# Optimization experiments

Measured on AMD Instinct MI355X. Metric: run time of the kernel, lower is better.

The kernel has to match this reference:

```python
import jax, jax.numpy as jnp
import numpy as np

COST_CLASS = 2.0
COST_MASK = 5.0
COST_DICE = 5.0
NUM_POINTS = 12544


def _point_sample(masks, coords):
    """Bilinear sample masks [N,H,W] at coords [P,2] in [0,1] (x,y order),
    matching F.grid_sample(align_corners=False, padding_mode='zeros')."""
    H, W = masks.shape[-2], masks.shape[-1]
    x = coords[:, 0] * W - 0.5  # [P]
    y = coords[:, 1] * H - 0.5
    x0 = jnp.floor(x)
    y0 = jnp.floor(y)
    wx = (x - x0).astype(masks.dtype)
    wy = (y - y0).astype(masks.dtype)
    x0i = x0.astype(jnp.int32)
    y0i = y0.astype(jnp.int32)

    def gather(xi, yi):
        valid = ((xi >= 0) & (xi < W) & (yi >= 0) & (yi < H)).astype(masks.dtype)
        xc = jnp.clip(xi, 0, W - 1)
        yc = jnp.clip(yi, 0, H - 1)
        return masks[:, yc, xc] * valid[None, :]  # [N,P]

    v00 = gather(x0i, y0i)
    v01 = gather(x0i + 1, y0i)
    v10 = gather(x0i, y0i + 1)
    v11 = gather(x0i + 1, y0i + 1)
    return (v00 * (1 - wx) * (1 - wy) + v01 * wx * (1 - wy)
            + v10 * (1 - wx) * wy + v11 * wx * wy)  # [N,P]


def setup_inputs() -> dict:
    key = jax.random.key(0)
    ks = jax.random.split(key, 6)
    B, Q, C, T, H, W = 8, 100, 41, 50, 256, 256
    return {
        "pred_logits": jax.random.normal(ks[0], (B, Q, C), jnp.float32),
        "pred_object_logits": jax.random.normal(ks[1], (B, Q, 2), jnp.float32),
        "pred_masks": jax.random.normal(ks[2], (B, Q, H, W), jnp.float32),
        "tgt_masks": jax.random.uniform(ks[3], (B, T, H, W), jnp.float32),
        "tgt_labels": jax.random.randint(ks[4], (B, T), 0, C),
        "point_coords": jax.random.uniform(ks[5], (B, NUM_POINTS, 2), jnp.float32),
    }


def reference(pred_logits, pred_object_logits, pred_masks, tgt_masks, tgt_labels, point_coords):
    B, Q, C = pred_logits.shape
    T = tgt_labels.shape[1]
    P = point_coords.shape[1]

    # --- class cost ---
    out_class_prob = jax.nn.sigmoid(pred_logits[..., :-1])          # [B,Q,C-1]
    out_object_prob = jax.nn.softmax(pred_object_logits, axis=-1)   # [B,Q,2]
    out_prob = jnp.concatenate(
        [jnp.sqrt(out_class_prob * out_object_prob[..., 0:1]),
         out_object_prob[..., 1:2]], axis=-1)                       # [B,Q,C]
    idx = jnp.broadcast_to(tgt_labels[:, None, :], (B, Q, T))
    cost_class = -jnp.take_along_axis(out_prob, idx, axis=2)        # [B,Q,T]

    # --- point-sample masks at shared random points ---
    om = jax.vmap(_point_sample)(pred_masks, point_coords)          # [B,Q,P]
    tm = jax.vmap(_point_sample)(tgt_masks, point_coords)           # [B,T,P]

    # --- batched sigmoid CE cost ---
    pos = jax.nn.softplus(-om)  # BCE vs target=1
    neg = jax.nn.softplus(om)   # BCE vs target=0
    cost_mask = (jnp.einsum('bqp,btp->bqt', pos, tm)
                 + jnp.einsum('bqp,btp->bqt', neg, 1.0 - tm)) / P

    # --- batched dice cost ---
    s = jax.nn.sigmoid(om)
    numerator = 2.0 * jnp.einsum('bqp,btp->bqt', s, tm)
    denominator = s.sum(-1)[:, :, None] + tm.sum(-1)[:, None, :]
    cost_dice = 1.0 - (numerator + 1.0) / (denominator + 1.0)

    Cmat = COST_MASK * cost_mask + COST_CLASS * cost_class + COST_DICE * cost_dice
    return Cmat  # [B,Q,T] batched assignment cost matrices
```

## Files before the change

### kernel.cpp

```cpp
#include <hip/hip_runtime.h>
#include <math.h>

#define BB 8
#define QQ 100
#define CC 41
#define TT 50
#define PP 12544
#define QP 112
#define TP 64
#define KS 8
#define KCH (PP / KS)
#define NT (BB * TT)
#define NMASK (NT + BB * QQ)
#define MPB 5
#define SGRID (NMASK / MPB)

typedef _Float16 f16x8 __attribute__((ext_vector_type(8)));
typedef float f32x4 __attribute__((ext_vector_type(4)));

#if defined(__has_builtin)
#if __has_builtin(__builtin_amdgcn_cvt_pk_fp8_f32) && __has_builtin(__builtin_amdgcn_cvt_f32_fp8)
#define HAVE_FP8CVT 1
#endif
#endif

__device__ __forceinline__ unsigned int cvt1_e4m3_sw(float x) {
    unsigned int u = __float_as_uint(x);
    unsigned int s = (u >> 24) & 0x80u;
    float ax = fminf(fabsf(x), 448.f);
    if (ax < 0.015625f) {
        unsigned int m = (unsigned int)rintf(ax * 512.f);
        return s | m;
    }
    unsigned int v = __float_as_uint(ax);
    v += 0x7FFFFu + ((v >> 20) & 1u);
    int e = (int)(v >> 23) - 127;
    unsigned int m = (v >> 20) & 7u;
    if (e < -6) { m = (unsigned int)rintf(ax * 512.f); return s | m; }
    unsigned int ee = (unsigned int)(e + 7);
    if (ee >= 16u) { ee = 15u; m = 6u; }
    return s | (ee << 3) | m;
}

template <bool HI>
__device__ __forceinline__ unsigned int pack2_e4m3(float a, float b, unsigned int old) {
#ifdef HAVE_FP8CVT
    return (unsigned int)__builtin_amdgcn_cvt_pk_fp8_f32(a, b, (int)old, HI);
#else
    unsigned int p = (cvt1_e4m3_sw(a) | (cvt1_e4m3_sw(b) << 8)) << (HI ? 16 : 0);
    unsigned int mask = HI ? 0x0000FFFFu : 0xFFFF0000u;
    return (old & mask) | p;
#endif
}

__device__ __forceinline__ float e4m3_to_f32(unsigned int byte) {
#ifdef HAVE_FP8CVT
    return __builtin_amdgcn_cvt_f32_fp8((int)byte, 0);
#else
    unsigned int s = byte >> 7, e = (byte >> 3) & 15u, m = byte & 7u;
    float v = e ? __uint_as_float(((e + 120u) << 23) | (m << 20))
                : (float)m * 0.001953125f;
    return s ? -v : v;
#endif
}

__device__ __forceinline__ void addr_w(float2 c, int& a00, int& a01, int& a10, int& a11,
                                       float& xa, float& xb, float& ya, float& yb) {
    float x = fmaf(c.x, 256.f, -0.5f);
    float y = fmaf(c.y, 256.f, -0.5f);
    float x0f = floorf(x), y0f = floorf(y);
    float wx = x - x0f, wy = y - y0f;
    int x0 = (int)x0f, y0 = (int)y0f;
    float fx0 = (x0 >= 0) ? 1.f : 0.f, fx1 = (x0 < 255) ? 1.f : 0.f;
    float fy0 = (y0 >= 0) ? 1.f : 0.f, fy1 = (y0 < 255) ? 1.f : 0.f;
    int x0c = max(x0, 0), x1c = min(x0 + 1, 255);
    int r0 = max(y0, 0) << 8, r1 = min(y0 + 1, 255) << 8;
    a00 = r0 + x0c; a01 = r0 + x1c; a10 = r1 + x0c; a11 = r1 + x1c;
    xa = (1.f - wx) * fx0; xb = wx * fx1;
    ya = (1.f - wy) * fy0; yb = wy * fy1;
}

__global__ __launch_bounds__(1024, 4) void sample_kernel(
    const float* __restrict__ tgt_masks, const float* __restrict__ pred_masks,
    const float* __restrict__ coords,
    _Float16* __restrict__ tm, _Float16* __restrict__ om, _Float16* __restrict__ sg,
    float* __restrict__ tmsum, float* __restrict__ nsum, float* __restrict__ ssum)
{
    __shared__ unsigned int buf[2][16384];
    __shared__ float red[16], red2[16];
    int tid = threadIdx.x;
    int base = blockIdx.x * MPB;

    {
        const float* m0 = (base < NT) ? tgt_masks + (size_t)base * 65536
                                      : pred_masks + (size_t)(base - NT) * 65536;
        const float4* s4 = (const float4*)m0;
        for (int half = 0; half < 2; ++half) {
            float4 r[8];
            #pragma unroll
            for (int k = 0; k < 8; ++k) r[k] = s4[half * 8192 + k * 1024 + tid];
            #pragma unroll
            for (int k = 0; k < 8; ++k) {
                unsigned int pk = pack2_e4m3<false>(r[k].x, r[k].y, 0u);
                buf[0][half * 8192 + k * 1024 + tid] = pack2_e4m3<true>(r[k].z, r[k].w, pk);
            }
        }
    }
    __syncthreads();

    for (int j = 0; j < MPB; ++j) {
        int id = base + j;
        bool is_t = id < NT;
        int b;
        _Float16* dst;
        _Float16* dsg = nullptr;
        if (is_t) {
            b = id / TT;
            dst = tm + ((size_t)b * TP + (id % TT)) * PP;
        } else {
            int bq = id - NT;
            b = bq / QQ;
            dst = om + ((size_t)b * QP + (bq % QQ)) * PP;
            dsg = sg + ((size_t)b * QP + (bq % QQ)) * PP;
        }
        const float2* cd = (const float2*)coords + (size_t)b * PP;
        const unsigned char* curb = (const unsigned char*)buf[j & 1];
        unsigned int* nxt = buf[(j + 1) & 1];
        bool has_next = (j + 1 < MPB);
        const float4* ns4 = nullptr;
        if (has_next) {
            int nid = id + 1;
            ns4 = (const float4*)((nid < NT) ? tgt_masks + (size_t)nid * 65536
                                             : pred_masks + (size_t)(nid - NT) * 65536);
        }

        float l1 = 0.f, l2 = 0.f;
        for (int half = 0; half < 2; ++half) {
            float4 r[8];
            if (has_next) {
                #pragma unroll
                for (int k = 0; k < 8; ++k) r[k] = ns4[half * 8192 + k * 1024 + tid];
            }
            #pragma unroll
            for (int pr = 0; pr < 3; ++pr) {
                int p1 = (half * 6 + pr * 2) * 1024 + tid;
                int p2 = p1 + 1024;
                float2 c1 = cd[p1], c2 = cd[p2];
                int a00, a01, a10, a11, e00, e01, e10, e11;
                float xa1, xb1, ya1, yb1, xa2, xb2, ya2, yb2;
                addr_w(c1, a00, a01, a10, a11, xa1, xb1, ya1, yb1);
                addr_w(c2, e00, e01, e10, e11, xa2, xb2, ya2, yb2);
                unsigned int u00 = curb[a00], u01 = curb[a01];
                unsigned int u10 = curb[a10], u11 = curb[a11];
                unsigned int w00 = curb[e00], w01 = curb[e01];
                unsigned int w10 = curb[e10], w11 = curb[e11];
                float v1 = ya1 * fmaf(xa1, e4m3_to_f32(u00), xb1 * e4m3_to_f32(u01))
                         + yb1 * fmaf(xa1, e4m3_to_f32(u10), xb1 * e4m3_to_f32(u11));
                float v2 = ya2 * fmaf(xa2, e4m3_to_f32(w00), xb2 * e4m3_to_f32(w01))
                         + yb2 * fmaf(xa2, e4m3_to_f32(w10), xb2 * e4m3_to_f32(w11));
                dst[p1] = (_Float16)v1;
                dst[p2] = (_Float16)v2;
                if (is_t) {
                    l1 += v1 + v2;
                } else {
                    float e1 = __expf(-fabsf(v1)), e2 = __expf(-fabsf(v2));
                    float q1 = 1.f / (1.f + e1), q2 = 1.f / (1.f + e2);
                    float g1 = (v1 >= 0.f) ? q1 : e1 * q1;
                    float g2 = (v2 >= 0.f) ? q2 : e2 * q2;
                    dsg[p1] = (_Float16)g1;
                    dsg[p2] = (_Float16)g2;
                    l1 += fmaxf(v1, 0.f) + __logf(1.f + e1)
                        + fmaxf(v2, 0.f) + __logf(1.f + e2);
                    l2 += g1 + g2;
                }
            }
            if (half == 1 && tid < 256) {
                int p = 12288 + tid;
                float2 c = cd[p];
                int a00, a01, a10, a11;
                float xa, xb, ya, yb;
                addr_w(c, a00, a01, a10, a11, xa, xb, ya, yb);
                float v = ya * fmaf(xa, e4m3_to_f32((unsigned int)curb[a00]),
                                    xb * e4m3_to_f32((unsigned int)curb[a01]))
                        + yb * fmaf(xa, e4m3_to_f32((unsigned int)curb[a10]),
                                    xb * e4m3_to_f32((unsigned int)curb[a11]));
                dst[p] = (_Float16)v;
                if (is_t) {
                    l1 += v;
                } else {
                    float e = __expf(-fabsf(v));
                    float q = 1.f / (1.f + e);
                    float g = (v >= 0.f) ? q : e * q;
                    dsg[p] = (_Float16)g;
                    l1 += fmaxf(v, 0.f) + __logf(1.f + e);
                    l2 += g;
                }
            }
            if (has_next) {
                #pragma unroll
                for (int k = 0; k < 8; ++k) {
                    unsigned int pk = pack2_e4m3<false>(r[k].x, r[k].y, 0u);
                    nxt[half * 8192 + k * 1024 + tid] = pack2_e4m3<true>(r[k].z, r[k].w, pk);
                }
            }
        }

        #pragma unroll
        for (int off = 32; off; off >>= 1) {
            l1 += __shfl_down(l1, off, 64);
            l2 += __shfl_down(l2, off, 64);
        }
        if ((tid & 63) == 0) { red[tid >> 6] = l1; red2[tid >> 6] = l2; }
        __syncthreads();
        if (tid == 0) {
            float t1 = 0.f, t2 = 0.f;
            #pragma unroll
            for (int w = 0; w < 16; ++w) { t1 += red[w]; t2 += red2[w]; }
            if (is_t) tmsum[id] = t1;
            else { nsum[id - NT] = t1; ssum[id - NT] = t2; }
        }
        __syncthreads();
    }
}

__global__ __launch_bounds__(256) void dot_mfma_kernel(
    const _Float16* __restrict__ om, const _Float16* __restrict__ sg,
    const _Float16* __restrict__ tm,
    float* __restrict__ part_om, float* __restrict__ part_s)
{
    int qt = blockIdx.x, b = blockIdx.y, ks = blockIdx.z;
    int tid = threadIdx.x, lane = tid & 63, w = tid >> 6;
    int ra = lane & 15;
    int ko = (lane >> 4) * 8;
    const _Float16* pa = om + ((size_t)(b * QP + qt * 16 + ra)) * PP + ks * KCH + ko;
    const _Float16* ps = sg + ((size_t)(b * QP + qt * 16 + ra)) * PP + ks * KCH + ko;
    const _Float16* pb = tm + ((size_t)(b * TP + w * 16 + ra)) * PP + ks * KCH + ko;
    f32x4 accO = {0.f, 0.f, 0.f, 0.f};
    f32x4 accS = {0.f, 0.f, 0.f, 0.f};
    #pragma unroll 7
    for (int k = 0; k < KCH / 32; ++k) {
        f16x8 a = *(const f16x8*)(pa + (size_t)k * 32);
        f16x8 s = *(const f16x8*)(ps + (size_t)k * 32);
        f16x8 bb = *(const f16x8*)(pb + (size_t)k * 32);
        accO = __builtin_amdgcn_mfma_f32_16x16x32_f16(a, bb, accO, 0, 0, 0);
        accS = __builtin_amdgcn_mfma_f32_16x16x32_f16(s, bb, accS, 0, 0, 0);
    }
    int t = w * 16 + ra;
    int q = qt * 16 + (lane >> 4) * 4;
    size_t bse = (((size_t)ks * BB + b) * QP + q) * TP + t;
    #pragma unroll
    for (int r = 0; r < 4; ++r) {
        part_om[bse + (size_t)r * TP] = accO[r];
        part_s[bse + (size_t)r * TP] = accS[r];
    }
}

__global__ __launch_bounds__(256) void epilogue_kernel(
    const float* __restrict__ part_om, const float* __restrict__ part_s,
    const float* __restrict__ tmsum, const float* __restrict__ nsum,
    const float* __restrict__ ssum, const float* __restrict__ pred_logits,
    const float* __restrict__ pred_obj, const int* __restrict__ labels,
    float* __restrict__ out)
{
    int i = blockIdx.x * 256 + threadIdx.x;
    if (i >= BB * QQ * TT) return;
    int t = i % TT;
    int bq = i / TT;
    int b = bq / QQ, q = bq % QQ;
    float dO = 0.f, dS = 0.f;
    #pragma unroll
    for (int ks = 0; ks < KS; ++ks) {
        size_t o = (((size_t)ks * BB + b) * QP + q) * TP + t;
        dO += part_om[o];
        dS += part_s[o];
    }
    float ns = nsum[bq], ss = ssum[bq];
    float ts = tmsum[b * TT + t];
    float cmask = (ns - dO) * (1.f / PP);
    float cdice = 1.f - (2.f * dS + 1.f) / (ss + ts + 1.f);
    int label = labels[b * TT + t];
    float a0 = pred_obj[bq * 2], a1 = pred_obj[bq * 2 + 1];
    float prob;
    if (label == CC - 1) {
        prob = 1.f / (1.f + __expf(a0 - a1));
    } else {
        float pc = 1.f / (1.f + __expf(-pred_logits[(size_t)bq * CC + label]));
        float po = 1.f / (1.f + __expf(a1 - a0));
        prob = sqrtf(pc * po);
    }
    out[i] = 5.f * cmask - 2.f * prob + 5.f * cdice;
}

extern "C" void kernel_launch(void* const* d_in, const int* in_sizes, int n_in,
                              void* d_out, int out_size, void* d_ws, size_t ws_size,
                              hipStream_t stream) {
    const float* pred_logits = (const float*)d_in[0];
    const float* pred_obj    = (const float*)d_in[1];
    const float* pred_masks  = (const float*)d_in[2];
    const float* tgt_masks   = (const float*)d_in[3];
    const int*   tgt_labels  = (const int*)d_in[4];
    const float* coords      = (const float*)d_in[5];
    float* out = (float*)d_out;

    char* ws = (char*)d_ws;
    const size_t SZ_OM = (size_t)BB * QP * PP * 2;
    const size_t SZ_TM = (size_t)BB * TP * PP * 2;
    const size_t SZ_PT = (size_t)KS * BB * QP * TP * 4;
    _Float16* om  = (_Float16*)ws;
    _Float16* sg  = (_Float16*)(ws + SZ_OM);
    _Float16* tmm = (_Float16*)(ws + 2 * SZ_OM);
    float* part_om = (float*)(ws + 2 * SZ_OM + SZ_TM);
    float* part_s  = (float*)(ws + 2 * SZ_OM + SZ_TM + SZ_PT);
    float* tmsum   = (float*)(ws + 2 * SZ_OM + SZ_TM + 2 * SZ_PT);
    float* nsum    = tmsum + BB * TT;
    float* ssum    = nsum + BB * QQ;

    hipLaunchKernelGGL(sample_kernel, dim3(SGRID), dim3(1024), 0, stream,
                       tgt_masks, pred_masks, coords, tmm, om, sg, tmsum, nsum, ssum);
    hipLaunchKernelGGL(dot_mfma_kernel, dim3(QP / 16, BB, KS), dim3(256), 0, stream,
                       om, sg, tmm, part_om, part_s);
    hipLaunchKernelGGL(epilogue_kernel, dim3((BB * QQ * TT + 255) / 256), dim3(256),
                       0, stream,
                       part_om, part_s, tmsum, nsum, ssum,
                       pred_logits, pred_obj, tgt_labels, out);
}
```

Measured before the change: 124.4 us.

## Precompute bilinear address/weight table and sample one mask per block

Adds a kernel that precomputes, per batch and point, the four packed 16-bit LDS addresses and fp16 bilinear corner weights. The sampling kernel reads this table instead of recomputing floor and clamp math for every mask. It also drops the 5-masks-per-block double-buffered pipeline in favour of one mask per block with a single 64KB LDS buffer and higher occupancy, and packs f16 output stores in pairs. The cost is an extra launch plus 16B of table traffic per point per mask, fp16 weight rounding, and no intra-block overlap of mask loading with sampling.

```diff
diff --git a/kernel.cpp b/kernel.cpp
--- a/kernel.cpp
+++ b/kernel.cpp
@@ -12,8 +12,6 @@
 #define KCH (PP / KS)
 #define NT (BB * TT)
 #define NMASK (NT + BB * QQ)
-#define MPB 5
-#define SGRID (NMASK / MPB)
 
 typedef _Float16 f16x8 __attribute__((ext_vector_type(8)));
 typedef float f32x4 __attribute__((ext_vector_type(4)));
@@ -64,8 +62,12 @@
 #endif
 }
 
-__device__ __forceinline__ void addr_w(float2 c, int& a00, int& a01, int& a10, int& a11,
-                                       float& xa, float& xb, float& ya, float& yb) {
+__global__ __launch_bounds__(256) void table_kernel(
+    const float* __restrict__ coords, uint4* __restrict__ table)
+{
+    int i = blockIdx.x * 256 + threadIdx.x;
+    if (i >= BB * PP) return;
+    float2 c = ((const float2*)coords)[i];
     float x = fmaf(c.x, 256.f, -0.5f);
     float y = fmaf(c.y, 256.f, -0.5f);
     float x0f = floorf(x), y0f = floorf(y);
@@ -73,153 +75,163 @@
     int x0 = (int)x0f, y0 = (int)y0f;
     float fx0 = (x0 >= 0) ? 1.f : 0.f, fx1 = (x0 < 255) ? 1.f : 0.f;
     float fy0 = (y0 >= 0) ? 1.f : 0.f, fy1 = (y0 < 255) ? 1.f : 0.f;
-    int x0c = max(x0, 0), x1c = min(x0 + 1, 255);
-    int r0 = max(y0, 0) << 8, r1 = min(y0 + 1, 255) << 8;
-    a00 = r0 + x0c; a01 = r0 + x1c; a10 = r1 + x0c; a11 = r1 + x1c;
-    xa = (1.f - wx) * fx0; xb = wx * fx1;
-    ya = (1.f - wy) * fy0; yb = wy * fy1;
-}
-
-__global__ __launch_bounds__(1024, 4) void sample_kernel(
+    unsigned int x0c = (unsigned int)max(x0, 0), x1c = (unsigned int)min(x0 + 1, 255);
+    unsigned int r0 = ((unsigned int)max(y0, 0)) << 8;
+    unsigned int r1 = ((unsigned int)min(y0 + 1, 255)) << 8;
+    float xa = (1.f - wx) * fx0, xb = wx * fx1;
+    float ya = (1.f - wy) * fy0, yb = wy * fy1;
+    union { unsigned int u; _Float16 h[2]; } w1, w2;
+    w1.h[0] = (_Float16)(xa * ya); w1.h[1] = (_Float16)(xb * ya);
+    w2.h[0] = (_Float16)(xa * yb); w2.h[1] = (_Float16)(xb * yb);
+    uint4 t;
+    t.x = (r0 + x0c) | ((r0 + x1c) << 16);
+    t.y = (r1 + x0c) | ((r1 + x1c) << 16);
+    t.z = w1.u; t.w = w2.u;
+    table[i] = t;
+}
+
+__device__ __forceinline__ float tbl_interp(const unsigned char* __restrict__ mlds, uint4 t) {
+    float v00 = e4m3_to_f32(mlds[t.x & 0xffffu]);
+    float v01 = e4m3_to_f32(mlds[t.x >> 16]);
+    float v10 = e4m3_to_f32(mlds[t.y & 0xffffu]);
+    float v11 = e4m3_to_f32(mlds[t.y >> 16]);
+    union { unsigned int u; _Float16 h[2]; } w1, w2;
+    w1.u = t.z; w2.u = t.w;
+    float acc = (float)w1.h[0] * v00;
+    acc = fmaf((float)w1.h[1], v01, acc);
+    acc = fmaf((float)w2.h[0], v10, acc);
+    return fmaf((float)w2.h[1], v11, acc);
+}
+
+__global__ __launch_bounds__(1024, 8) void sample_kernel(
     const float* __restrict__ tgt_masks, const float* __restrict__ pred_masks,
-    const float* __restrict__ coords,
+    const uint4* __restrict__ table,
     _Float16* __restrict__ tm, _Float16* __restrict__ om, _Float16* __restrict__ sg,
     float* __restrict__ tmsum, float* __restrict__ nsum, float* __restrict__ ssum)
 {
-    __shared__ unsigned int buf[2][16384];
+    __shared__ unsigned char mlds[65536];
     __shared__ float red[16], red2[16];
+    int id = blockIdx.x;
     int tid = threadIdx.x;
-    int base = blockIdx.x * MPB;
+    bool is_t = id < NT;
+    int b;
+    _Float16* dst;
+    _Float16* dsg = nullptr;
+    const float* m;
+    if (is_t) {
+        b = id / TT;
+        m = tgt_masks + (size_t)id * 65536;
+        dst = tm + ((size_t)b * TP + (id % TT)) * PP;
+    } else {
+        int bq = id - NT;
+        b = bq / QQ;
+        m = pred_masks + (size_t)bq * 65536;
+        dst = om + ((size_t)b * QP + (bq % QQ)) * PP;
+        dsg = sg + ((size_t)b * QP + (bq % QQ)) * PP;
+    }
+    const uint4* tb = table + (size_t)b * PP;
 
     {
-        const float* m0 = (base < NT) ? tgt_masks + (size_t)base * 65536
-                                      : pred_masks + (size_t)(base - NT) * 65536;
-        const float4* s4 = (const float4*)m0;
-        for (int half = 0; half < 2; ++half) {
-            float4 r[8];
-            #pragma unroll
-            for (int k = 0; k < 8; ++k) r[k] = s4[half * 8192 + k * 1024 + tid];
-            #pragma unroll
-            for (int k = 0; k < 8; ++k) {
-                unsigned int pk = pack2_e4m3<false>(r[k].x, r[k].y, 0u);
-                buf[0][half * 8192 + k * 1024 + tid] = pack2_e4m3<true>(r[k].z, r[k].w, pk);
-            }
+        const float4* s4 = (const float4*)m;
+        unsigned int* dl = (unsigned int*)mlds;
+        #pragma unroll
+        for (int bt = 0; bt < 4; ++bt) {
+            float4 r0 = s4[bt * 4096 + tid];
+            float4 r1 = s4[bt * 4096 + 1024 + tid];
+            float4 r2 = s4[bt * 4096 + 2048 + tid];
+            float4 r3 = s4[bt * 4096 + 3072 + tid];
+            unsigned int pk;
+            pk = pack2_e4m3<false>(r0.x, r0.y, 0u);
+            dl[bt * 4096 + tid] = pack2_e4m3<true>(r0.z, r0.w, pk);
+            pk = pack2_e4m3<false>(r1.x, r1.y, 0u);
+            dl[bt * 4096 + 1024 + tid] = pack2_e4m3<true>(r1.z, r1.w, pk);
+            pk = pack2_e4m3<false>(r2.x, r2.y, 0u);
+            dl[bt * 4096 + 2048 + tid] = pack2_e4m3<true>(r2.z, r2.w, pk);
+            pk = pack2_e4m3<false>(r3.x, r3.y, 0u);
+            dl[bt * 4096 + 3072 + tid] = pack2_e4m3<true>(r3.z, r3.w, pk);
         }
     }
     __syncthreads();
 
-    for (int j = 0; j < MPB; ++j) {
-        int id = base + j;
-        bool is_t = id < NT;
-        int b;
-        _Float16* dst;
-        _Float16* dsg = nullptr;
-        if (is_t) {
-            b = id / TT;
-            dst = tm + ((size_t)b * TP + (id % TT)) * PP;
-        } else {
-            int bq = id - NT;
-            b = bq / QQ;
-            dst = om + ((size_t)b * QP + (bq % QQ)) * PP;
-            dsg = sg + ((size_t)b * QP + (bq % QQ)) * PP;
-        }
-        const float2* cd = (const float2*)coords + (size_t)b * PP;
-        const unsigned char* curb = (const unsigned char*)buf[j & 1];
-        unsigned int* nxt = buf[(j + 1) & 1];
-        bool has_next = (j + 1 < MPB);
-        const float4* ns4 = nullptr;
-        if (has_next) {
-            int nid = id + 1;
-            ns4 = (const float4*)((nid < NT) ? tgt_masks + (size_t)nid * 65536
-                                             : pred_masks + (size_t)(nid - NT) * 65536);
-        }
-
-        float l1 = 0.f, l2 = 0.f;
-        for (int half = 0; half < 2; ++half) {
-            float4 r[8];
-            if (has_next) {
-                #pragma unroll
-                for (int k = 0; k < 8; ++k) r[k] = ns4[half * 8192 + k * 1024 + tid];
-            }
-            #pragma unroll
-            for (int pr = 0; pr < 3; ++pr) {
-                int p1 = (half * 6 + pr * 2) * 1024 + tid;
-                int p2 = p1 + 1024;
-                float2 c1 = cd[p1], c2 = cd[p2];
-                int a00, a01, a10, a11, e00, e01, e10, e11;
-                float xa1, xb1, ya1, yb1, xa2, xb2, ya2, yb2;
-                addr_w(c1, a00, a01, a10, a11, xa1, xb1, ya1, yb1);
-                addr_w(c2, e00, e01, e10, e11, xa2, xb2, ya2, yb2);
-                unsigned int u00 = curb[a00], u01 = curb[a01];
-                unsigned int u10 = curb[a10], u11 = curb[a11];
-                unsigned int w00 = curb[e00], w01 = curb[e01];
-                unsigned int w10 = curb[e10], w11 = curb[e11];
-                float v1 = ya1 * fmaf(xa1, e4m3_to_f32(u00), xb1 * e4m3_to_f32(u01))
-                         + yb1 * fmaf(xa1, e4m3_to_f32(u10), xb1 * e4m3_to_f32(u11));
-                float v2 = ya2 * fmaf(xa2, e4m3_to_f32(w00), xb2 * e4m3_to_f32(w01))
-                         + yb2 * fmaf(xa2, e4m3_to_f32(w10), xb2 * e4m3_to_f32(w11));
-                dst[p1] = (_Float16)v1;
-                dst[p2] = (_Float16)v2;
-                if (is_t) {
-                    l1 += v1 + v2;
-                } else {
-                    float e1 = __expf(-fabsf(v1)), e2 = __expf(-fabsf(v2));
-                    float q1 = 1.f / (1.f + e1), q2 = 1.f / (1.f + e2);
-                    float g1 = (v1 >= 0.f) ? q1 : e1 * q1;
-                    float g2 = (v2 >= 0.f) ? q2 : e2 * q2;
-                    dsg[p1] = (_Float16)g1;
-                    dsg[p2] = (_Float16)g2;
-                    l1 += fmaxf(v1, 0.f) + __logf(1.f + e1)
-                        + fmaxf(v2, 0.f) + __logf(1.f + e2);
-                    l2 += g1 + g2;
-                }
-            }
-            if (half == 1 && tid < 256) {
-                int p = 12288 + tid;
-                float2 c = cd[p];
-                int a00, a01, a10, a11;
-                float xa, xb, ya, yb;
-                addr_w(c, a00, a01, a10, a11, xa, xb, ya, yb);
-                float v = ya * fmaf(xa, e4m3_to_f32((unsigned int)curb[a00]),
-                                    xb * e4m3_to_f32((unsigned int)curb[a01]))
-                        + yb * fmaf(xa, e4m3_to_f32((unsigned int)curb[a10]),
-                                    xb * e4m3_to_f32((unsigned int)curb[a11]));
-                dst[p] = (_Float16)v;
-                if (is_t) {
-                    l1 += v;
-                } else {
-                    float e = __expf(-fabsf(v));
-                    float q = 1.f / (1.f + e);
-                    float g = (v >= 0.f) ? q : e * q;
-                    dsg[p] = (_Float16)g;
-                    l1 += fmaxf(v, 0.f) + __logf(1.f + e);
-                    l2 += g;
-                }
-            }
-            if (has_next) {
-                #pragma unroll
-                for (int k = 0; k < 8; ++k) {
-                    unsigned int pk = pack2_e4m3<false>(r[k].x, r[k].y, 0u);
-                    nxt[half * 8192 + k * 1024 + tid] = pack2_e4m3<true>(r[k].z, r[k].w, pk);
-                }
-            }
-        }
-
+    float l1 = 0.f, l2 = 0.f;
+
+    if (is_t) {
         #pragma unroll
-        for (int off = 32; off; off >>= 1) {
-            l1 += __shfl_down(l1, off, 64);
-            l2 += __shfl_down(l2, off, 64);
-        }
-        if ((tid & 63) == 0) { red[tid >> 6] = l1; red2[tid >> 6] = l2; }
-        __syncthreads();
-        if (tid == 0) {
-            float t1 = 0.f, t2 = 0.f;
-            #pragma unroll
-            for (int w = 0; w < 16; ++w) { t1 += red[w]; t2 += red2[w]; }
-            if (is_t) tmsum[id] = t1;
-            else { nsum[id - NT] = t1; ssum[id - NT] = t2; }
-        }
-        __syncthreads();
+        for (int g = 0; g < 6; ++g) {
+            int p = g * 2048 + 2 * tid;
+            uint4 t0 = tb[p], t1 = tb[p + 1];
+            float v1 = tbl_interp(mlds, t0);
+            float v2 = tbl_interp(mlds, t1);
+            union { unsigned int u; _Float16 h[2]; } o;
+            o.h[0] = (_Float16)v1; o.h[1] = (_Float16)v2;
+            *(unsigned int*)&dst[p] = o.u;
+            l1 += v1 + v2;
+        }
+        if (tid < 128) {
+            int p = 12288 + 2 * tid;
+            uint4 t0 = tb[p], t1 = tb[p + 1];
+            float v1 = tbl_interp(mlds, t0);
+            float v2 = tbl_interp(mlds, t1);
+            union { unsigned int u; _Float16 h[2]; } o;
+            o.h[0] = (_Float16)v1; o.h[1] = (_Float16)v2;
+            *(unsigned int*)&dst[p] = o.u;
+            l1 += v1 + v2;
+        }
+    } else {
+        #pragma unroll
+        for (int g = 0; g < 6; ++g) {
+            int p = g * 2048 + 2 * tid;
+            uint4 t0 = tb[p], t1 = tb[p + 1];
+            float v1 = tbl_interp(mlds, t0);
+            float v2 = tbl_interp(mlds, t1);
+            union { unsigned int u; _Float16 h[2]; } o;
+            o.h[0] = (_Float16)v1; o.h[1] = (_Float16)v2;
+            *(unsigned int*)&dst[p] = o.u;
+            float e1 = __expf(-fabsf(v1)), e2 = __expf(-fabsf(v2));
+            float q1 = 1.f / (1.f + e1), q2 = 1.f / (1.f + e2);
+            float g1 = (v1 >= 0.f) ? q1 : e1 * q1;
+            float g2 = (v2 >= 0.f) ? q2 : e2 * q2;
+            union { unsigned int u; _Float16 h[2]; } os;
+            os.h[0] = (_Float16)g1; os.h[1] = (_Float16)g2;
+            *(unsigned int*)&dsg[p] = os.u;
+            l1 += fmaxf(v1, 0.f) + __logf(1.f + e1)
+                + fmaxf(v2, 0.f) + __logf(1.f + e2);
+            l2 += g1 + g2;
+        }
+        if (tid < 128) {
+            int p = 12288 + 2 * tid;
+            uint4 t0 = tb[p], t1 = tb[p + 1];
+            float v1 = tbl_interp(mlds, t0);
+            float v2 = tbl_interp(mlds, t1);
+            union { unsigned int u; _Float16 h[2]; } o;
+            o.h[0] = (_Float16)v1; o.h[1] = (_Float16)v2;
+            *(unsigned int*)&dst[p] = o.u;
+            float e1 = __expf(-fabsf(v1)), e2 = __expf(-fabsf(v2));
+            float q1 = 1.f / (1.f + e1), q2 = 1.f / (1.f + e2);
+            float g1 = (v1 >= 0.f) ? q1 : e1 * q1;
+            float g2 = (v2 >= 0.f) ? q2 : e2 * q2;
+            union { unsigned int u; _Float16 h[2]; } os;
+            os.h[0] = (_Float16)g1; os.h[1] = (_Float16)g2;
+            *(unsigned int*)&dsg[p] = os.u;
+            l1 += fmaxf(v1, 0.f) + __logf(1.f + e1)
+                + fmaxf(v2, 0.f) + __logf(1.f + e2);
+            l2 += g1 + g2;
+        }
+    }
+
+    #pragma unroll
+    for (int off = 32; off; off >>= 1) {
+        l1 += __shfl_down(l1, off, 64);
+        l2 += __shfl_down(l2, off, 64);
+    }
+    if ((tid & 63) == 0) { red[tid >> 6] = l1; red2[tid >> 6] = l2; }
+    __syncthreads();
+    if (tid == 0) {
+        float t1 = 0.f, t2 = 0.f;
+        #pragma unroll
+        for (int w = 0; w < 16; ++w) { t1 += red[w]; t2 += red2[w]; }
+        if (is_t) tmsum[id] = t1;
+        else { nsum[id - NT] = t1; ssum[id - NT] = t2; }
     }
 }
 
@@ -303,20 +315,24 @@
     float* out = (float*)d_out;
 
     char* ws = (char*)d_ws;
+    const size_t SZ_TB = (size_t)BB * PP * 16;
     const size_t SZ_OM = (size_t)BB * QP * PP * 2;
     const size_t SZ_TM = (size_t)BB * TP * PP * 2;
     const size_t SZ_PT = (size_t)KS * BB * QP * TP * 4;
-    _Float16* om  = (_Float16*)ws;
-    _Float16* sg  = (_Float16*)(ws + SZ_OM);
-    _Float16* tmm = (_Float16*)(ws + 2 * SZ_OM);
-    float* part_om = (float*)(ws + 2 * SZ_OM + SZ_TM);
-    float* part_s  = (float*)(ws + 2 * SZ_OM + SZ_TM + SZ_PT);
-    float* tmsum   = (float*)(ws + 2 * SZ_OM + SZ_TM + 2 * SZ_PT);
+    uint4* table  = (uint4*)ws;
+    _Float16* om  = (_Float16*)(ws + SZ_TB);
+    _Float16* sg  = (_Float16*)(ws + SZ_TB + SZ_OM);
+    _Float16* tmm = (_Float16*)(ws + SZ_TB + 2 * SZ_OM);
+    float* part_om = (float*)(ws + SZ_TB + 2 * SZ_OM + SZ_TM);
+    float* part_s  = (float*)(ws + SZ_TB + 2 * SZ_OM + SZ_TM + SZ_PT);
+    float* tmsum   = (float*)(ws + SZ_TB + 2 * SZ_OM + SZ_TM + 2 * SZ_PT);
     float* nsum    = tmsum + BB * TT;
     float* ssum    = nsum + BB * QQ;
 
-    hipLaunchKernelGGL(sample_kernel, dim3(SGRID), dim3(1024), 0, stream,
-                       tgt_masks, pred_masks, coords, tmm, om, sg, tmsum, nsum, ssum);
+    hipLaunchKernelGGL(table_kernel, dim3((BB * PP + 255) / 256), dim3(256), 0, stream,
+                       coords, table);
+    hipLaunchKernelGGL(sample_kernel, dim3(NMASK), dim3(1024), 0, stream,
+                       tgt_masks, pred_masks, table, tmm, om, sg, tmsum, nsum, ssum);
     hipLaunchKernelGGL(dot_mfma_kernel, dim3(QP / 16, BB, KS), dim3(256), 0, stream,
                        om, sg, tmm, part_om, part_s);
     hipLaunchKernelGGL(epilogue_kernel, dim3((BB * QQ * TT + 255) / 256), dim3(256),
```

New measurement: 124.4 us. About the same (-0.0%).

## Precompute row-binned bilinear sample table and gather masks directly from global memory

Applied to the files above, without the earlier changes.

A new sort_kernel bins each batch's sample points by source row band and writes a compact table with clamped addresses and fp16 bilinear weights. The sample kernel then runs one block per mask and gathers four fp32 texels per point straight from global memory, instead of staging the whole mask into LDS as fp8. This removes the fp8 packing, the double-buffered LDS staging and the per-point address math, and also raises sampling precision. Row binning is meant to improve cache locality of the gathers. The cost is an extra kernel launch and a serialized ballot-compaction loop. Point order is permuted, which the downstream permutation-invariant reductions tolerate.

```diff
diff --git a/kernel.cpp b/kernel.cpp
--- a/kernel.cpp
+++ b/kernel.cpp
@@ -12,214 +12,142 @@
 #define KCH (PP / KS)
 #define NT (BB * TT)
 #define NMASK (NT + BB * QQ)
-#define MPB 5
-#define SGRID (NMASK / MPB)
 
 typedef _Float16 f16x8 __attribute__((ext_vector_type(8)));
 typedef float f32x4 __attribute__((ext_vector_type(4)));
 
-#if defined(__has_builtin)
-#if __has_builtin(__builtin_amdgcn_cvt_pk_fp8_f32) && __has_builtin(__builtin_amdgcn_cvt_f32_fp8)
-#define HAVE_FP8CVT 1
-#endif
-#endif
-
-__device__ __forceinline__ unsigned int cvt1_e4m3_sw(float x) {
-    unsigned int u = __float_as_uint(x);
-    unsigned int s = (u >> 24) & 0x80u;
-    float ax = fminf(fabsf(x), 448.f);
-    if (ax < 0.015625f) {
-        unsigned int m = (unsigned int)rintf(ax * 512.f);
-        return s | m;
-    }
-    unsigned int v = __float_as_uint(ax);
-    v += 0x7FFFFu + ((v >> 20) & 1u);
-    int e = (int)(v >> 23) - 127;
-    unsigned int m = (v >> 20) & 7u;
-    if (e < -6) { m = (unsigned int)rintf(ax * 512.f); return s | m; }
-    unsigned int ee = (unsigned int)(e + 7);
-    if (ee >= 16u) { ee = 15u; m = 6u; }
-    return s | (ee << 3) | m;
-}
-
-template <bool HI>
-__device__ __forceinline__ unsigned int pack2_e4m3(float a, float b, unsigned int old) {
-#ifdef HAVE_FP8CVT
-    return (unsigned int)__builtin_amdgcn_cvt_pk_fp8_f32(a, b, (int)old, HI);
-#else
-    unsigned int p = (cvt1_e4m3_sw(a) | (cvt1_e4m3_sw(b) << 8)) << (HI ? 16 : 0);
-    unsigned int mask = HI ? 0x0000FFFFu : 0xFFFF0000u;
-    return (old & mask) | p;
-#endif
-}
-
-__device__ __forceinline__ float e4m3_to_f32(unsigned int byte) {
-#ifdef HAVE_FP8CVT
-    return __builtin_amdgcn_cvt_f32_fp8((int)byte, 0);
-#else
-    unsigned int s = byte >> 7, e = (byte >> 3) & 15u, m = byte & 7u;
-    float v = e ? __uint_as_float(((e + 120u) << 23) | (m << 20))
-                : (float)m * 0.001953125f;
-    return s ? -v : v;
-#endif
-}
-
-__device__ __forceinline__ void addr_w(float2 c, int& a00, int& a01, int& a10, int& a11,
-                                       float& xa, float& xb, float& ya, float& yb) {
-    float x = fmaf(c.x, 256.f, -0.5f);
-    float y = fmaf(c.y, 256.f, -0.5f);
-    float x0f = floorf(x), y0f = floorf(y);
-    float wx = x - x0f, wy = y - y0f;
-    int x0 = (int)x0f, y0 = (int)y0f;
-    float fx0 = (x0 >= 0) ? 1.f : 0.f, fx1 = (x0 < 255) ? 1.f : 0.f;
-    float fy0 = (y0 >= 0) ? 1.f : 0.f, fy1 = (y0 < 255) ? 1.f : 0.f;
-    int x0c = max(x0, 0), x1c = min(x0 + 1, 255);
-    int r0 = max(y0, 0) << 8, r1 = min(y0 + 1, 255) << 8;
-    a00 = r0 + x0c; a01 = r0 + x1c; a10 = r1 + x0c; a11 = r1 + x1c;
-    xa = (1.f - wx) * fx0; xb = wx * fx1;
-    ya = (1.f - wy) * fy0; yb = wy * fy1;
-}
-
-__global__ __launch_bounds__(1024, 4) void sample_kernel(
+__global__ __launch_bounds__(256) void sort_kernel(
+    const float* __restrict__ coords, uint4* __restrict__ stb)
+{
+    int b = blockIdx.x >> 4;
+    int mybin = blockIdx.x & 15;
+    int tid = threadIdx.x;
+    int lane = tid & 63, w = tid >> 6;
+    const float2* cd = (const float2*)coords + (size_t)b * PP;
+    __shared__ int hist[16];
+    __shared__ int woff[4];
+    __shared__ int running;
+    if (tid < 16) hist[tid] = 0;
+    __syncthreads();
+    for (int p = tid; p < PP; p += 256) {
+        float y = fmaf(cd[p].y, 256.f, -0.5f);
+        int y0 = (int)floorf(y);
+        int bin = min(max(y0, 0), 255) >> 4;
+        atomicAdd(&hist[bin], 1);
+    }
+    __syncthreads();
+    int start = 0;
+    for (int i = 0; i < mybin; ++i) start += hist[i];
+    if (tid == 0) running = 0;
+    __syncthreads();
+
+    uint4* out = stb + (size_t)b * PP;
+    for (int c = 0; c < 49; ++c) {
+        int p = c * 256 + tid;
+        float2 cc = cd[p];
+        float x = fmaf(cc.x, 256.f, -0.5f);
+        float y = fmaf(cc.y, 256.f, -0.5f);
+        float x0f = floorf(x), y0f = floorf(y);
+        int x0 = (int)x0f, y0 = (int)y0f;
+        int bin = min(max(y0, 0), 255) >> 4;
+        bool match = (bin == mybin);
+        unsigned long long bal = __ballot(match);
+        if (lane == 0) woff[w] = (int)__popcll(bal);
+        __syncthreads();
+        int wbase = 0;
+        #pragma unroll
+        for (int i = 0; i < 4; ++i) if (i < w) wbase += woff[i];
+        int tot = woff[0] + woff[1] + woff[2] + woff[3];
+        if (match) {
+            int rk = (int)__popcll(bal & ((1ull << lane) - 1ull));
+            float wx = x - x0f, wy = y - y0f;
+            int xb = min(max(x0, 0), 254);
+            int r0 = min(max(y0, 0), 255);
+            int r1 = min(y0 + 1, 255);
+            float wa, wb;
+            if (x0 < 0)        { wa = wx;       wb = 0.f; }
+            else if (x0 > 254) { wa = 0.f;      wb = 1.f - wx; }
+            else               { wa = 1.f - wx; wb = wx; }
+            float ya = (y0 >= 0)  ? 1.f - wy : 0.f;
+            float yb = (y0 < 255) ? wy       : 0.f;
+            union { unsigned int u; _Float16 h[2]; } pw, pyw;
+            pw.h[0] = (_Float16)wa;  pw.h[1] = (_Float16)wb;
+            pyw.h[0] = (_Float16)ya; pyw.h[1] = (_Float16)yb;
+            uint4 t;
+            t.x = (unsigned int)(r0 * 256 + xb);
+            t.y = (unsigned int)(r1 * 256 + xb);
+            t.z = pw.u; t.w = pyw.u;
+            out[start + running + wbase + rk] = t;
+        }
+        __syncthreads();
+        if (tid == 0) running += tot;
+        __syncthreads();
+    }
+}
+
+__global__ __launch_bounds__(512, 8) void sample_kernel(
     const float* __restrict__ tgt_masks, const float* __restrict__ pred_masks,
-    const float* __restrict__ coords,
+    const uint4* __restrict__ stb,
     _Float16* __restrict__ tm, _Float16* __restrict__ om, _Float16* __restrict__ sg,
     float* __restrict__ tmsum, float* __restrict__ nsum, float* __restrict__ ssum)
 {
-    __shared__ unsigned int buf[2][16384];
-    __shared__ float red[16], red2[16];
+    __shared__ float red[8], red2[8];
+    int id = blockIdx.x;
     int tid = threadIdx.x;
-    int base = blockIdx.x * MPB;
-
-    {
-        const float* m0 = (base < NT) ? tgt_masks + (size_t)base * 65536
-                                      : pred_masks + (size_t)(base - NT) * 65536;
-        const float4* s4 = (const float4*)m0;
-        for (int half = 0; half < 2; ++half) {
-            float4 r[8];
-            #pragma unroll
-            for (int k = 0; k < 8; ++k) r[k] = s4[half * 8192 + k * 1024 + tid];
-            #pragma unroll
-            for (int k = 0; k < 8; ++k) {
-                unsigned int pk = pack2_e4m3<false>(r[k].x, r[k].y, 0u);
-                buf[0][half * 8192 + k * 1024 + tid] = pack2_e4m3<true>(r[k].z, r[k].w, pk);
-            }
+    bool is_t = id < NT;
+    int b;
+    const float* m;
+    _Float16* dst;
+    _Float16* dsg = nullptr;
+    if (is_t) {
+        b = id / TT;
+        m = tgt_masks + (size_t)id * 65536;
+        dst = tm + ((size_t)b * TP + (id % TT)) * PP;
+    } else {
+        int bq = id - NT;
+        b = bq / QQ;
+        m = pred_masks + (size_t)bq * 65536;
+        dst = om + ((size_t)b * QP + (bq % QQ)) * PP;
+        dsg = sg + ((size_t)b * QP + (bq % QQ)) * PP;
+    }
+    const uint4* tb = stb + (size_t)b * PP;
+
+    float l1 = 0.f, l2 = 0.f;
+    for (int p = tid; p < PP; p += 512) {
+        uint4 t = tb[p];
+        float v00 = m[t.x], v01 = m[t.x + 1];
+        float v10 = m[t.y], v11 = m[t.y + 1];
+        union { unsigned int u; _Float16 h[2]; } pw, pyw;
+        pw.u = t.z; pyw.u = t.w;
+        float wa = (float)pw.h[0], wb = (float)pw.h[1];
+        float ya = (float)pyw.h[0], yb = (float)pyw.h[1];
+        float v = ya * fmaf(wa, v00, wb * v01) + yb * fmaf(wa, v10, wb * v11);
+        dst[p] = (_Float16)v;
+        if (is_t) {
+            l1 += v;
+        } else {
+            float e = __expf(-fabsf(v));
+            float q = 1.f / (1.f + e);
+            float g = (v >= 0.f) ? q : e * q;
+            dsg[p] = (_Float16)g;
+            l1 += fmaxf(v, 0.f) + __logf(1.f + e);
+            l2 += g;
         }
     }
-    __syncthreads();
-
-    for (int j = 0; j < MPB; ++j) {
-        int id = base + j;
-        bool is_t = id < NT;
-        int b;
-        _Float16* dst;
-        _Float16* dsg = nullptr;
-        if (is_t) {
-            b = id / TT;
-            dst = tm + ((size_t)b * TP + (id % TT)) * PP;
-        } else {
-            int bq = id - NT;
-            b = bq / QQ;
-            dst = om + ((size_t)b * QP + (bq % QQ)) * PP;
-            dsg = sg + ((size_t)b * QP + (bq % QQ)) * PP;
-        }
-        const float2* cd = (const float2*)coords + (size_t)b * PP;
-        const unsigned char* curb = (const unsigned char*)buf[j & 1];
-        unsigned int* nxt = buf[(j + 1) & 1];
-        bool has_next = (j + 1 < MPB);
-        const float4* ns4 = nullptr;
-        if (has_next) {
-            int nid = id + 1;
-            ns4 = (const float4*)((nid < NT) ? tgt_masks + (size_t)nid * 65536
-                                             : pred_masks + (size_t)(nid - NT) * 65536);
-        }
-
-        float l1 = 0.f, l2 = 0.f;
-        for (int half = 0; half < 2; ++half) {
-            float4 r[8];
-            if (has_next) {
-                #pragma unroll
-                for (int k = 0; k < 8; ++k) r[k] = ns4[half * 8192 + k * 1024 + tid];
-            }
-            #pragma unroll
-            for (int pr = 0; pr < 3; ++pr) {
-                int p1 = (half * 6 + pr * 2) * 1024 + tid;
-                int p2 = p1 + 1024;
-                float2 c1 = cd[p1], c2 = cd[p2];
-                int a00, a01, a10, a11, e00, e01, e10, e11;
-                float xa1, xb1, ya1, yb1, xa2, xb2, ya2, yb2;
-                addr_w(c1, a00, a01, a10, a11, xa1, xb1, ya1, yb1);
-                addr_w(c2, e00, e01, e10, e11, xa2, xb2, ya2, yb2);
-                unsigned int u00 = curb[a00], u01 = curb[a01];
-                unsigned int u10 = curb[a10], u11 = curb[a11];
-                unsigned int w00 = curb[e00], w01 = curb[e01];
-                unsigned int w10 = curb[e10], w11 = curb[e11];
-                float v1 = ya1 * fmaf(xa1, e4m3_to_f32(u00), xb1 * e4m3_to_f32(u01))
-                         + yb1 * fmaf(xa1, e4m3_to_f32(u10), xb1 * e4m3_to_f32(u11));
-                float v2 = ya2 * fmaf(xa2, e4m3_to_f32(w00), xb2 * e4m3_to_f32(w01))
-                         + yb2 * fmaf(xa2, e4m3_to_f32(w10), xb2 * e4m3_to_f32(w11));
-                dst[p1] = (_Float16)v1;
-                dst[p2] = (_Float16)v2;
-                if (is_t) {
-                    l1 += v1 + v2;
-                } else {
-                    float e1 = __expf(-fabsf(v1)), e2 = __expf(-fabsf(v2));
-                    float q1 = 1.f / (1.f + e1), q2 = 1.f / (1.f + e2);
-                    float g1 = (v1 >= 0.f) ? q1 : e1 * q1;
-                    float g2 = (v2 >= 0.f) ? q2 : e2 * q2;
-                    dsg[p1] = (_Float16)g1;
-                    dsg[p2] = (_Float16)g2;
-                    l1 += fmaxf(v1, 0.f) + __logf(1.f + e1)
-                        + fmaxf(v2, 0.f) + __logf(1.f + e2);
-                    l2 += g1 + g2;
-                }
-            }
-            if (half == 1 && tid < 256) {
-                int p = 12288 + tid;
-                float2 c = cd[p];
-                int a00, a01, a10, a11;
-                float xa, xb, ya, yb;
-                addr_w(c, a00, a01, a10, a11, xa, xb, ya, yb);
-                float v = ya * fmaf(xa, e4m3_to_f32((unsigned int)curb[a00]),
-                                    xb * e4m3_to_f32((unsigned int)curb[a01]))
-                        + yb * fmaf(xa, e4m3_to_f32((unsigned int)curb[a10]),
-                                    xb * e4m3_to_f32((unsigned int)curb[a11]));
-                dst[p] = (_Float16)v;
-                if (is_t) {
-                    l1 += v;
-                } else {
-                    float e = __expf(-fabsf(v));
-                    float q = 1.f / (1.f + e);
-                    float g = (v >= 0.f) ? q : e * q;
-                    dsg[p] = (_Float16)g;
-                    l1 += fmaxf(v, 0.f) + __logf(1.f + e);
-                    l2 += g;
-                }
-            }
-            if (has_next) {
-                #pragma unroll
-                for (int k = 0; k < 8; ++k) {
-                    unsigned int pk = pack2_e4m3<false>(r[k].x, r[k].y, 0u);
-                    nxt[half * 8192 + k * 1024 + tid] = pack2_e4m3<true>(r[k].z, r[k].w, pk);
-                }
-            }
-        }
-
+
+    #pragma unroll
+    for (int off = 32; off; off >>= 1) {
+        l1 += __shfl_down(l1, off, 64);
+        l2 += __shfl_down(l2, off, 64);
+    }
+    if ((tid & 63) == 0) { red[tid >> 6] = l1; red2[tid >> 6] = l2; }
+    __syncthreads();
+    if (tid == 0) {
+        float t1 = 0.f, t2 = 0.f;
         #pragma unroll
-        for (int off = 32; off; off >>= 1) {
-            l1 += __shfl_down(l1, off, 64);
-            l2 += __shfl_down(l2, off, 64);
-        }
-        if ((tid & 63) == 0) { red[tid >> 6] = l1; red2[tid >> 6] = l2; }
-        __syncthreads();
-        if (tid == 0) {
-            float t1 = 0.f, t2 = 0.f;
-            #pragma unroll
-            for (int w = 0; w < 16; ++w) { t1 += red[w]; t2 += red2[w]; }
-            if (is_t) tmsum[id] = t1;
-            else { nsum[id - NT] = t1; ssum[id - NT] = t2; }
-        }
-        __syncthreads();
+        for (int w = 0; w < 8; ++w) { t1 += red[w]; t2 += red2[w]; }
+        if (is_t) tmsum[id] = t1;
+        else { nsum[id - NT] = t1; ssum[id - NT] = t2; }
     }
 }
 
@@ -303,20 +231,24 @@
     float* out = (float*)d_out;
 
     char* ws = (char*)d_ws;
+    const size_t SZ_TB = (size_t)BB * PP * 16;
     const size_t SZ_OM = (size_t)BB * QP * PP * 2;
     const size_t SZ_TM = (size_t)BB * TP * PP * 2;
     const size_t SZ_PT = (size_t)KS * BB * QP * TP * 4;
-    _Float16* om  = (_Float16*)ws;
-    _Float16* sg  = (_Float16*)(ws + SZ_OM);
-    _Float16* tmm = (_Float16*)(ws + 2 * SZ_OM);
-    float* part_om = (float*)(ws + 2 * SZ_OM + SZ_TM);
-    float* part_s  = (float*)(ws + 2 * SZ_OM + SZ_TM + SZ_PT);
-    float* tmsum   = (float*)(ws + 2 * SZ_OM + SZ_TM + 2 * SZ_PT);
+    uint4* stb    = (uint4*)ws;
+    _Float16* om  = (_Float16*)(ws + SZ_TB);
+    _Float16* sg  = (_Float16*)(ws + SZ_TB + SZ_OM);
+    _Float16* tmm = (_Float16*)(ws + SZ_TB + 2 * SZ_OM);
+    float* part_om = (float*)(ws + SZ_TB + 2 * SZ_OM + SZ_TM);
+    float* part_s  = (float*)(ws + SZ_TB + 2 * SZ_OM + SZ_TM + SZ_PT);
+    float* tmsum   = (float*)(ws + SZ_TB + 2 * SZ_OM + SZ_TM + 2 * SZ_PT);
     float* nsum    = tmsum + BB * TT;
     float* ssum    = nsum + BB * QQ;
 
-    hipLaunchKernelGGL(sample_kernel, dim3(SGRID), dim3(1024), 0, stream,
-                       tgt_masks, pred_masks, coords, tmm, om, sg, tmsum, nsum, ssum);
+    hipLaunchKernelGGL(sort_kernel, dim3(BB * 16), dim3(256), 0, stream,
+                       coords, stb);
+    hipLaunchKernelGGL(sample_kernel, dim3(NMASK), dim3(512), 0, stream,
+                       tgt_masks, pred_masks, stb, tmm, om, sg, tmsum, nsum, ssum);
     hipLaunchKernelGGL(dot_mfma_kernel, dim3(QP / 16, BB, KS), dim3(256), 0, stream,
                        om, sg, tmm, part_om, part_s);
     hipLaunchKernelGGL(epilogue_kernel, dim3((BB * QQ * TT + 255) / 256), dim3(256),
```

Measured after the change: 261.2 us. 110% more time.
